# Performance work log

Measured on AMD Instinct MI355X. Metric: run time of the kernel, lower is better.

The kernel has to match this reference:

```python
import jax, jax.numpy as jnp
import numpy as np

B, S, D = 4, 2048, 1024
H = 16
HD = D // H  # head dim = 64


def setup_inputs() -> dict:
    key = jax.random.key(0)
    ks = jax.random.split(key, 9)
    s = 1.0 / np.sqrt(D)
    return {
        "Q": jax.random.normal(ks[0], (B, S, D), dtype=jnp.float32),
        "K": jax.random.normal(ks[1], (B, S, D), dtype=jnp.float32),
        "V": jax.random.normal(ks[2], (B, S, D), dtype=jnp.float32),
        "Wq": jax.random.uniform(ks[3], (D, D), jnp.float32, -s, s),
        "bq": jax.random.uniform(ks[4], (D,), jnp.float32, -s, s),
        "Wk": jax.random.uniform(ks[5], (D, D), jnp.float32, -s, s),
        "bk": jax.random.uniform(ks[6], (D,), jnp.float32, -s, s),
        "Wv": jax.random.uniform(ks[7], (D, D), jnp.float32, -s, s),
        "bv": jax.random.uniform(ks[8], (D,), jnp.float32, -s, s),
    }


def reference(Q, K, V, Wq, bq, Wk, bk, Wv, bv):
    # Linear projections, split into heads: (B, H, S, HD)
    def proj(x, W, b):
        y = x @ W + b  # torch Linear uses x @ W.T; here W is stored pre-transposed (D_in, D_out)
        return y.reshape(B, S, H, HD).transpose(0, 2, 1, 3)

    q = proj(Q, Wq, bq)
    k = proj(K, Wk, bk)
    v = proj(V, Wv, bv)

    scale = 1.0 / jnp.sqrt(jnp.float32(HD))
    scores = jnp.einsum("bhqd,bhkd->bhqk", q, k) * scale  # (B,H,S,S)
    # causal mask (mask=True path): -inf above the diagonal
    causal = jnp.triu(jnp.full((S, S), -jnp.inf, dtype=scores.dtype), k=1)
    scores = scores + causal
    attn = jax.nn.softmax(scores, axis=-1)
    ctx = jnp.einsum("bhqk,bhkd->bhqd", attn, v)  # (B,H,S,HD)
    return ctx.transpose(0, 2, 1, 3).reshape(B, S, H * HD)
```

## Files before the change

### kernel.cpp

```cpp
#include <hip/hip_runtime.h>
#include <hip/hip_bf16.h>
#include <stdint.h>

#define B_  4
#define S_  2048
#define D_  1024
#define H_  16
#define HD_ 64
#define LOG2E 1.44269504088896f

typedef unsigned short u16;
typedef short bf16x8 __attribute__((ext_vector_type(8)));
typedef float f32x4 __attribute__((ext_vector_type(4)));

static __device__ __forceinline__ u16 f2bf(float f) {
    union { float f; uint32_t u; } v; v.f = f;
    return (u16)((v.u + 0x7FFF + ((v.u >> 16) & 1)) >> 16);
}

static __device__ __forceinline__ uint32_t cvt_pk_bf16(float lo, float hi) {
    uint32_t r;
    asm("v_cvt_pk_bf16_f32 %0, %1, %2" : "=v"(r) : "v"(lo), "v"(hi));
    return r;
}

static __device__ __forceinline__ uint32_t pk2(float lo, float hi) {
    return __builtin_amdgcn_perm(__float_as_uint(hi), __float_as_uint(lo), 0x07060302u);
}

static __device__ __forceinline__ bf16x8 rd_swz(const u16* base, int row, int slot) {
    return *(const bf16x8*)((const char*)base + row * 128 + ((slot ^ (row & 7)) << 4));
}

static __device__ __forceinline__ void gll_swz(const u16* grow0, size_t stride,
                                               u16* lds_chunk, int lane) {
    const int r = lane >> 3;
    const int slot = (lane & 7) ^ r;
    const u16* g = grow0 + (size_t)r * stride + slot * 8;
    __builtin_amdgcn_global_load_lds(
        (const __attribute__((address_space(1))) uint32_t*)g,
        (__attribute__((address_space(3))) uint32_t*)lds_chunk, 16, 0, 0);
}

__global__ __launch_bounds__(256) void wtrans(
    const float* __restrict__ W0, const float* __restrict__ W1, const float* __restrict__ W2,
    u16* __restrict__ T0, u16* __restrict__ T1, u16* __restrict__ T2)
{
    const float* W = blockIdx.z == 0 ? W0 : (blockIdx.z == 1 ? W1 : W2);
    u16* T       = blockIdx.z == 0 ? T0 : (blockIdx.z == 1 ? T1 : T2);
    __shared__ float t[32][33];
    const int n0 = blockIdx.x * 32, k0 = blockIdx.y * 32;
    const int tx = threadIdx.x, ty = threadIdx.y;
#pragma unroll
    for (int i = 0; i < 4; ++i)
        t[ty + i * 8][tx] = W[(size_t)(k0 + ty + i * 8) * D_ + n0 + tx];
    __syncthreads();
#pragma unroll
    for (int i = 0; i < 4; ++i)
        T[(size_t)(n0 + ty + i * 8) * D_ + k0 + tx] = f2bf(t[tx][ty + i * 8]);
}

template <int MODE>
__global__ __launch_bounds__(256) void proj_gemm(
    const float* __restrict__ X, const u16* __restrict__ Wt,
    const float* __restrict__ bias, u16* __restrict__ out)
{
    __shared__ __align__(16) u16 lA[128 * 64];
    __shared__ __align__(16) u16 lB[128 * 64];
    const int tid = threadIdx.x;
    const int m0 = blockIdx.x * 128, n0 = blockIdx.y * 128;
    const int w = tid >> 6, lane = tid & 63;
    const int lr = lane & 15, lg = lane >> 4;
    const int wr = (w >> 1) * 64, wc = (w & 1) * 64;

    f32x4 acc[4][4] = {};

    for (int k0 = 0; k0 < D_; k0 += 64) {
        __syncthreads();
#pragma unroll
        for (int i = 0; i < 4; ++i) {
            const int c = w * 4 + i;
            gll_swz(Wt + (size_t)(n0 + c * 8) * D_ + k0, D_, &lB[c * 512], lane);
        }
#pragma unroll
        for (int i = 0; i < 8; ++i) {
            const int lin = i * 1024 + tid * 4;
            const int r = lin >> 6, c = lin & 63;
            const float4 v = *(const float4*)(X + (size_t)(m0 + r) * D_ + k0 + c);
            uint2 pk;
            pk.x = pk2(v.x, v.y);
            pk.y = pk2(v.z, v.w);
            const int phys = r * 128 + (((c >> 3) ^ (r & 7)) << 4) + ((c & 7) << 1);
            *(uint2*)((char*)lA + phys) = pk;
        }
        __syncthreads();
#pragma unroll
        for (int kk = 0; kk < 64; kk += 32) {
            bf16x8 af[4], bfr[4];
#pragma unroll
            for (int m = 0; m < 4; ++m)
                af[m] = rd_swz(lA, wr + m * 16 + lr, (kk >> 3) + lg);
#pragma unroll
            for (int n = 0; n < 4; ++n)
                bfr[n] = rd_swz(lB, wc + n * 16 + lr, (kk >> 3) + lg);
#pragma unroll
            for (int m = 0; m < 4; ++m)
#pragma unroll
                for (int n = 0; n < 4; ++n)
                    acc[m][n] = __builtin_amdgcn_mfma_f32_16x16x32_bf16(af[m], bfr[n], acc[m][n], 0, 0, 0);
        }
    }
#pragma unroll
    for (int m = 0; m < 4; ++m)
#pragma unroll
        for (int n = 0; n < 4; ++n)
#pragma unroll
            for (int j = 0; j < 4; ++j) {
                const int gm = m0 + wr + m * 16 + lg * 4 + j;
                const int gn = n0 + wc + n * 16 + lr;
                float y = acc[m][n][j] + bias[gn];
                if (MODE == 0) y *= 0.125f * LOG2E;
                const int bb = gm >> 11, s = gm & (S_ - 1);
                const int h = gn >> 6, hd = gn & 63;
                size_t off;
                if (MODE < 2) off = (((size_t)bb * H_ + h) * S_ + s) * HD_ + hd;
                else {
                    const int s6 = s & 63;
                    const int sp = (s & ~63) | (s6 & 0x20) | ((s6 & 0xC) << 1) |
                                   ((s6 & 0x10) >> 2) | (s6 & 3);
                    off = (((size_t)bb * H_ + h) * HD_ + hd) * S_ + sp;
                }
                out[off] = f2bf(y);
            }
}

__global__ __launch_bounds__(512) void attn_kernel(
    const u16* __restrict__ qb, const u16* __restrict__ kb,
    const u16* __restrict__ vtb, float* __restrict__ out)
{
    const int bh = blockIdx.y;
    const int b = bh >> 4, h = bh & 15;
    const int tid = threadIdx.x;
    const int w = tid >> 6, lane = tid & 63;
    const int lr = lane & 15, lg = lane >> 4;

    __shared__ __align__(16) u16 lK0[64 * 64];
    __shared__ __align__(16) u16 lV0[64 * 64];
    __shared__ __align__(16) u16 lK1[64 * 64];
    __shared__ __align__(16) u16 lV1[64 * 64];

    const size_t kbase = (size_t)bh * S_ * HD_;
    const size_t vbase = (size_t)bh * HD_ * S_;

    union { uint32_t u[4]; bf16x8 v; } onesf;
    onesf.u[0] = onesf.u[1] = onesf.u[2] = onesf.u[3] = 0x3F803F80u;

    for (int e = 0; e < 2; ++e) {
        const int qi = (e == 0) ? (int)blockIdx.x : 15 - (int)blockIdx.x;
        const int q0 = qi * 128;
        const int qrow = q0 + w * 16 + lr;

        const size_t qoff = ((size_t)bh * S_ + qrow) * HD_;
        const bf16x8 qf0 = *(const bf16x8*)(qb + qoff + lg * 8);
        const bf16x8 qf1 = *(const bf16x8*)(qb + qoff + 32 + lg * 8);

        f32x4 oacc[4] = {};
        f32x4 lacc = {};

        const int tmax = 2 * qi + 1;

        auto compute = [&](int t, const u16* lK, const u16* lV) {
            const int kv0 = t * 64;
            f32x4 sacc[4];
            __builtin_amdgcn_s_setprio(1);
#pragma unroll
            for (int n = 0; n < 4; ++n) {
                const bf16x8 k0f = rd_swz(lK, n * 16 + lr, lg);
                const bf16x8 k1f = rd_swz(lK, n * 16 + lr, 4 + lg);
                f32x4 z = {};
                z = __builtin_amdgcn_mfma_f32_16x16x32_bf16(k0f, qf0, z, 0, 0, 0);
                z = __builtin_amdgcn_mfma_f32_16x16x32_bf16(k1f, qf1, z, 0, 0, 0);
                sacc[n] = z;
            }
            __builtin_amdgcn_s_setprio(0);

            if (t >= tmax - 1) {
#pragma unroll
                for (int n = 0; n < 4; ++n)
#pragma unroll
                    for (int j = 0; j < 4; ++j)
                        if (kv0 + n * 16 + lg * 4 + j > qrow) sacc[n][j] = -1e30f;
            }

            uint32_t pw[4][2];
#pragma unroll
            for (int n = 0; n < 4; ++n)
#pragma unroll
                for (int jh = 0; jh < 2; ++jh)
                    pw[n][jh] = cvt_pk_bf16(exp2f(sacc[n][2 * jh]),
                                            exp2f(sacc[n][2 * jh + 1]));

            union { uint32_t u[4]; bf16x8 v; } a0, a1;
            a0.u[0] = pw[0][0]; a0.u[1] = pw[0][1];
            a0.u[2] = pw[1][0]; a0.u[3] = pw[1][1];
            a1.u[0] = pw[2][0]; a1.u[1] = pw[2][1];
            a1.u[2] = pw[3][0]; a1.u[3] = pw[3][1];

            __builtin_amdgcn_s_setprio(1);
#pragma unroll
            for (int n = 0; n < 4; ++n) {
                const int row = n * 16 + lr;
                const bf16x8 vf0 = rd_swz(lV, row, lg);
                const bf16x8 vf1 = rd_swz(lV, row, 4 + lg);
                oacc[n] = __builtin_amdgcn_mfma_f32_16x16x32_bf16(a0.v, vf0, oacc[n], 0, 0, 0);
                oacc[n] = __builtin_amdgcn_mfma_f32_16x16x32_bf16(a1.v, vf1, oacc[n], 0, 0, 0);
            }
            lacc = __builtin_amdgcn_mfma_f32_16x16x32_bf16(a0.v, onesf.v, lacc, 0, 0, 0);
            lacc = __builtin_amdgcn_mfma_f32_16x16x32_bf16(a1.v, onesf.v, lacc, 0, 0, 0);
            __builtin_amdgcn_s_setprio(0);
        };

        for (int tp = 0; tp <= tmax; tp += 2) {
            const int kvA = tp * 64, kvB = kvA + 64;
            __syncthreads();
            gll_swz(kb + kbase + (size_t)(kvA + w * 8) * HD_, HD_, &lK0[w * 512], lane);
            gll_swz(vtb + vbase + (size_t)(w * 8) * S_ + kvA, S_, &lV0[w * 512], lane);
            gll_swz(kb + kbase + (size_t)(kvB + w * 8) * HD_, HD_, &lK1[w * 512], lane);
            gll_swz(vtb + vbase + (size_t)(w * 8) * S_ + kvB, S_, &lV1[w * 512], lane);
            __syncthreads();

            compute(tp, lK0, lV0);
            if (!(tp + 1 == tmax && w < 4)) compute(tp + 1, lK1, lV1);
        }

        f32x4 inv;
#pragma unroll
        for (int j = 0; j < 4; ++j) inv[j] = 1.f / lacc[j];
#pragma unroll
        for (int j = 0; j < 4; ++j) {
            const int row = q0 + w * 16 + lg * 4 + j;
#pragma unroll
            for (int n = 0; n < 4; ++n)
                out[((size_t)b * S_ + row) * D_ + h * HD_ + n * 16 + lr] = oacc[n][j] * inv[j];
        }
    }
}

extern "C" void kernel_launch(void* const* d_in, const int* in_sizes, int n_in,
                              void* d_out, int out_size, void* d_ws, size_t ws_size,
                              hipStream_t stream) {
    const float* Q  = (const float*)d_in[0];
    const float* K  = (const float*)d_in[1];
    const float* V  = (const float*)d_in[2];
    const float* Wq = (const float*)d_in[3];
    const float* bq = (const float*)d_in[4];
    const float* Wk = (const float*)d_in[5];
    const float* bk = (const float*)d_in[6];
    const float* Wv = (const float*)d_in[7];
    const float* bv = (const float*)d_in[8];
    float* out = (float*)d_out;

    char* ws = (char*)d_ws;
    const size_t WT_BYTES  = (size_t)D_ * D_ * 2;
    const size_t QKV_BYTES = (size_t)B_ * S_ * D_ * 2;
    u16* Wtq = (u16*)(ws);
    u16* Wtk = (u16*)(ws + WT_BYTES);
    u16* Wtv = (u16*)(ws + 2 * WT_BYTES);
    u16* qb  = (u16*)(ws + 3 * WT_BYTES);
    u16* kb  = (u16*)(ws + 3 * WT_BYTES + QKV_BYTES);
    u16* vtb = (u16*)(ws + 3 * WT_BYTES + 2 * QKV_BYTES);

    wtrans<<<dim3(32, 32, 3), dim3(32, 8), 0, stream>>>(Wq, Wk, Wv, Wtq, Wtk, Wtv);
    proj_gemm<0><<<dim3(64, 8), dim3(256), 0, stream>>>(Q, Wtq, bq, qb);
    proj_gemm<1><<<dim3(64, 8), dim3(256), 0, stream>>>(K, Wtk, bk, kb);
    proj_gemm<2><<<dim3(64, 8), dim3(256), 0, stream>>>(V, Wtv, bv, vtb);
    attn_kernel<<<dim3(8, B_ * H_), dim3(512), 0, stream>>>(qb, kb, vtb, out);
}
```

Measured before the change: 154.9 us.

## Double-buffer LDS in projection GEMM and attention to overlap loads with MFMA

Both the projection GEMM and the attention kernel now use two LDS buffers. The next K-tile (or KV pair) is prefetched while the current one is computed, which removes one barrier per iteration. In the GEMM, the fp32 activations are held in registers and converted to bf16 into the alternate buffer after the MFMAs. This costs twice the LDS (64KB per block in both kernels) and more VGPRs, which may lower occupancy. Correctness depends on the gll_swz async loads being waited on before the single barrier.

```diff
diff --git a/kernel.cpp b/kernel.cpp
--- a/kernel.cpp
+++ b/kernel.cpp
@@ -65,8 +65,8 @@
     const float* __restrict__ X, const u16* __restrict__ Wt,
     const float* __restrict__ bias, u16* __restrict__ out)
 {
-    __shared__ __align__(16) u16 lA[128 * 64];
-    __shared__ __align__(16) u16 lB[128 * 64];
+    __shared__ __align__(16) u16 lA[2][128 * 64];
+    __shared__ __align__(16) u16 lB[2][128 * 64];
     const int tid = threadIdx.x;
     const int m0 = blockIdx.x * 128, n0 = blockIdx.y * 128;
     const int w = tid >> 6, lane = tid & 63;
@@ -74,42 +74,69 @@
     const int wr = (w >> 1) * 64, wc = (w & 1) * 64;
 
     f32x4 acc[4][4] = {};
-
-    for (int k0 = 0; k0 < D_; k0 += 64) {
-        __syncthreads();
-#pragma unroll
-        for (int i = 0; i < 4; ++i) {
-            const int c = w * 4 + i;
-            gll_swz(Wt + (size_t)(n0 + c * 8) * D_ + k0, D_, &lB[c * 512], lane);
-        }
+    float4 areg[8];
+
+    auto loadA = [&](int k0) {
 #pragma unroll
         for (int i = 0; i < 8; ++i) {
             const int lin = i * 1024 + tid * 4;
             const int r = lin >> 6, c = lin & 63;
-            const float4 v = *(const float4*)(X + (size_t)(m0 + r) * D_ + k0 + c);
+            areg[i] = *(const float4*)(X + (size_t)(m0 + r) * D_ + k0 + c);
+        }
+    };
+    auto writeA = [&](u16* dst) {
+#pragma unroll
+        for (int i = 0; i < 8; ++i) {
+            const int lin = i * 1024 + tid * 4;
+            const int r = lin >> 6, c = lin & 63;
             uint2 pk;
-            pk.x = pk2(v.x, v.y);
-            pk.y = pk2(v.z, v.w);
+            pk.x = pk2(areg[i].x, areg[i].y);
+            pk.y = pk2(areg[i].z, areg[i].w);
             const int phys = r * 128 + (((c >> 3) ^ (r & 7)) << 4) + ((c & 7) << 1);
-            *(uint2*)((char*)lA + phys) = pk;
-        }
-        __syncthreads();
-#pragma unroll
-        for (int kk = 0; kk < 64; kk += 32) {
+            *(uint2*)((char*)dst + phys) = pk;
+        }
+    };
+    auto stageB = [&](int k0, u16* dst) {
+#pragma unroll
+        for (int i = 0; i < 4; ++i) {
+            const int c = w * 4 + i;
+            gll_swz(Wt + (size_t)(n0 + c * 8) * D_ + k0, D_, dst + c * 512, lane);
+        }
+    };
+    auto mfmaStep = [&](const u16* A, const u16* Bb) {
+#pragma unroll
+        for (int kk = 0; kk < 2; ++kk) {
             bf16x8 af[4], bfr[4];
 #pragma unroll
             for (int m = 0; m < 4; ++m)
-                af[m] = rd_swz(lA, wr + m * 16 + lr, (kk >> 3) + lg);
+                af[m] = rd_swz(A, wr + m * 16 + lr, kk * 4 + lg);
 #pragma unroll
             for (int n = 0; n < 4; ++n)
-                bfr[n] = rd_swz(lB, wc + n * 16 + lr, (kk >> 3) + lg);
+                bfr[n] = rd_swz(Bb, wc + n * 16 + lr, kk * 4 + lg);
 #pragma unroll
             for (int m = 0; m < 4; ++m)
 #pragma unroll
                 for (int n = 0; n < 4; ++n)
                     acc[m][n] = __builtin_amdgcn_mfma_f32_16x16x32_bf16(af[m], bfr[n], acc[m][n], 0, 0, 0);
         }
+    };
+
+    loadA(0);
+    stageB(0, lB[0]);
+    writeA(lA[0]);
+    __syncthreads();
+
+    for (int k0 = 0, s = 0; k0 < D_; k0 += 64, s ^= 1) {
+        const int nk = k0 + 64;
+        if (nk < D_) {
+            loadA(nk);
+            stageB(nk, lB[s ^ 1]);
+        }
+        mfmaStep(lA[s], lB[s]);
+        if (nk < D_) writeA(lA[s ^ 1]);
+        __syncthreads();
     }
+
 #pragma unroll
     for (int m = 0; m < 4; ++m)
 #pragma unroll
@@ -120,13 +147,13 @@
                 const int gn = n0 + wc + n * 16 + lr;
                 float y = acc[m][n][j] + bias[gn];
                 if (MODE == 0) y *= 0.125f * LOG2E;
-                const int bb = gm >> 11, s = gm & (S_ - 1);
+                const int bb = gm >> 11, s2 = gm & (S_ - 1);
                 const int h = gn >> 6, hd = gn & 63;
                 size_t off;
-                if (MODE < 2) off = (((size_t)bb * H_ + h) * S_ + s) * HD_ + hd;
+                if (MODE < 2) off = (((size_t)bb * H_ + h) * S_ + s2) * HD_ + hd;
                 else {
-                    const int s6 = s & 63;
-                    const int sp = (s & ~63) | (s6 & 0x20) | ((s6 & 0xC) << 1) |
+                    const int s6 = s2 & 63;
+                    const int sp = (s2 & ~63) | (s6 & 0x20) | ((s6 & 0xC) << 1) |
                                    ((s6 & 0x10) >> 2) | (s6 & 3);
                     off = (((size_t)bb * H_ + h) * HD_ + hd) * S_ + sp;
                 }
@@ -144,10 +171,7 @@
     const int w = tid >> 6, lane = tid & 63;
     const int lr = lane & 15, lg = lane >> 4;
 
-    __shared__ __align__(16) u16 lK0[64 * 64];
-    __shared__ __align__(16) u16 lV0[64 * 64];
-    __shared__ __align__(16) u16 lK1[64 * 64];
-    __shared__ __align__(16) u16 lV1[64 * 64];
+    __shared__ __align__(16) u16 lds[2][4][64 * 64];
 
     const size_t kbase = (size_t)bh * S_ * HD_;
     const size_t vbase = (size_t)bh * HD_ * S_;
@@ -168,6 +192,15 @@
         f32x4 lacc = {};
 
         const int tmax = 2 * qi + 1;
+
+        auto stage = [&](int tp, int s) {
+            const int kvA = tp * 64, kvB = kvA + 64;
+            u16* d = &lds[s][0][0];
+            gll_swz(kb + kbase + (size_t)(kvA + w * 8) * HD_, HD_, d + w * 512, lane);
+            gll_swz(vtb + vbase + (size_t)(w * 8) * S_ + kvA, S_, d + 4096 + w * 512, lane);
+            gll_swz(kb + kbase + (size_t)(kvB + w * 8) * HD_, HD_, d + 8192 + w * 512, lane);
+            gll_swz(vtb + vbase + (size_t)(w * 8) * S_ + kvB, S_, d + 12288 + w * 512, lane);
+        };
 
         auto compute = [&](int t, const u16* lK, const u16* lV) {
             const int kv0 = t * 64;
@@ -220,17 +253,15 @@
             __builtin_amdgcn_s_setprio(0);
         };
 
-        for (int tp = 0; tp <= tmax; tp += 2) {
-            const int kvA = tp * 64, kvB = kvA + 64;
+        stage(0, 0);
+        __syncthreads();
+
+        for (int tp = 0, s = 0; tp <= tmax; tp += 2, s ^= 1) {
+            if (tp + 2 <= tmax) stage(tp + 2, s ^ 1);
+            const u16* base = &lds[s][0][0];
+            compute(tp, base, base + 4096);
+            if (!(tp + 1 == tmax && w < 4)) compute(tp + 1, base + 8192, base + 12288);
             __syncthreads();
-            gll_swz(kb + kbase + (size_t)(kvA + w * 8) * HD_, HD_, &lK0[w * 512], lane);
-            gll_swz(vtb + vbase + (size_t)(w * 8) * S_ + kvA, S_, &lV0[w * 512], lane);
-            gll_swz(kb + kbase + (size_t)(kvB + w * 8) * HD_, HD_, &lK1[w * 512], lane);
-            gll_swz(vtb + vbase + (size_t)(w * 8) * S_ + kvB, S_, &lV1[w * 512], lane);
-            __syncthreads();
-
-            compute(tp, lK0, lV0);
-            if (!(tp + 1 == tmax && w < 4)) compute(tp + 1, lK1, lV1);
         }
 
         f32x4 inv;
```

Result: faster. 150.8 us (-2.7%).

## Double-buffer attention K/V staging and enlarge projection GEMM M tile

Applied to the files above, without the earlier changes.

The attention kernel now uses two LDS stages so the next pair of K/V tiles is loaded while the current pair is computed, with a single barrier per iteration. The goal is to hide global-to-LDS load latency that the old load-sync-compute loop exposed. The projection GEMM tile grows from 128 to 256 rows, giving 8x4 accumulators per wave and halving the grid. That improves weight-tile reuse but raises register pressure and leaves only 256 blocks per projection, which may underfill the GPU.

```diff
diff --git a/kernel.cpp b/kernel.cpp
--- a/kernel.cpp
+++ b/kernel.cpp
@@ -65,15 +65,15 @@
     const float* __restrict__ X, const u16* __restrict__ Wt,
     const float* __restrict__ bias, u16* __restrict__ out)
 {
-    __shared__ __align__(16) u16 lA[128 * 64];
+    __shared__ __align__(16) u16 lA[256 * 64];
     __shared__ __align__(16) u16 lB[128 * 64];
     const int tid = threadIdx.x;
-    const int m0 = blockIdx.x * 128, n0 = blockIdx.y * 128;
+    const int m0 = blockIdx.x * 256, n0 = blockIdx.y * 128;
     const int w = tid >> 6, lane = tid & 63;
     const int lr = lane & 15, lg = lane >> 4;
-    const int wr = (w >> 1) * 64, wc = (w & 1) * 64;
-
-    f32x4 acc[4][4] = {};
+    const int wr = (w >> 1) * 128, wc = (w & 1) * 64;
+
+    f32x4 acc[8][4] = {};
 
     for (int k0 = 0; k0 < D_; k0 += 64) {
         __syncthreads();
@@ -83,7 +83,7 @@
             gll_swz(Wt + (size_t)(n0 + c * 8) * D_ + k0, D_, &lB[c * 512], lane);
         }
 #pragma unroll
-        for (int i = 0; i < 8; ++i) {
+        for (int i = 0; i < 16; ++i) {
             const int lin = i * 1024 + tid * 4;
             const int r = lin >> 6, c = lin & 63;
             const float4 v = *(const float4*)(X + (size_t)(m0 + r) * D_ + k0 + c);
@@ -95,23 +95,23 @@
         }
         __syncthreads();
 #pragma unroll
-        for (int kk = 0; kk < 64; kk += 32) {
-            bf16x8 af[4], bfr[4];
-#pragma unroll
-            for (int m = 0; m < 4; ++m)
-                af[m] = rd_swz(lA, wr + m * 16 + lr, (kk >> 3) + lg);
+        for (int kk = 0; kk < 2; ++kk) {
+            bf16x8 af[8], bfr[4];
+#pragma unroll
+            for (int m = 0; m < 8; ++m)
+                af[m] = rd_swz(lA, wr + m * 16 + lr, kk * 4 + lg);
 #pragma unroll
             for (int n = 0; n < 4; ++n)
-                bfr[n] = rd_swz(lB, wc + n * 16 + lr, (kk >> 3) + lg);
-#pragma unroll
-            for (int m = 0; m < 4; ++m)
+                bfr[n] = rd_swz(lB, wc + n * 16 + lr, kk * 4 + lg);
+#pragma unroll
+            for (int m = 0; m < 8; ++m)
 #pragma unroll
                 for (int n = 0; n < 4; ++n)
                     acc[m][n] = __builtin_amdgcn_mfma_f32_16x16x32_bf16(af[m], bfr[n], acc[m][n], 0, 0, 0);
         }
     }
 #pragma unroll
-    for (int m = 0; m < 4; ++m)
+    for (int m = 0; m < 8; ++m)
 #pragma unroll
         for (int n = 0; n < 4; ++n)
 #pragma unroll
@@ -120,13 +120,13 @@
                 const int gn = n0 + wc + n * 16 + lr;
                 float y = acc[m][n][j] + bias[gn];
                 if (MODE == 0) y *= 0.125f * LOG2E;
-                const int bb = gm >> 11, s = gm & (S_ - 1);
+                const int bb = gm >> 11, s2 = gm & (S_ - 1);
                 const int h = gn >> 6, hd = gn & 63;
                 size_t off;
-                if (MODE < 2) off = (((size_t)bb * H_ + h) * S_ + s) * HD_ + hd;
+                if (MODE < 2) off = (((size_t)bb * H_ + h) * S_ + s2) * HD_ + hd;
                 else {
-                    const int s6 = s & 63;
-                    const int sp = (s & ~63) | (s6 & 0x20) | ((s6 & 0xC) << 1) |
+                    const int s6 = s2 & 63;
+                    const int sp = (s2 & ~63) | (s6 & 0x20) | ((s6 & 0xC) << 1) |
                                    ((s6 & 0x10) >> 2) | (s6 & 3);
                     off = (((size_t)bb * H_ + h) * HD_ + hd) * S_ + sp;
                 }
@@ -144,10 +144,7 @@
     const int w = tid >> 6, lane = tid & 63;
     const int lr = lane & 15, lg = lane >> 4;
 
-    __shared__ __align__(16) u16 lK0[64 * 64];
-    __shared__ __align__(16) u16 lV0[64 * 64];
-    __shared__ __align__(16) u16 lK1[64 * 64];
-    __shared__ __align__(16) u16 lV1[64 * 64];
+    __shared__ __align__(16) u16 lds[2][4][64 * 64];
 
     const size_t kbase = (size_t)bh * S_ * HD_;
     const size_t vbase = (size_t)bh * HD_ * S_;
@@ -168,6 +165,15 @@
         f32x4 lacc = {};
 
         const int tmax = 2 * qi + 1;
+
+        auto stage = [&](int tp, int s) {
+            const int kvA = tp * 64, kvB = kvA + 64;
+            u16* d = &lds[s][0][0];
+            gll_swz(kb + kbase + (size_t)(kvA + w * 8) * HD_, HD_, d + w * 512, lane);
+            gll_swz(vtb + vbase + (size_t)(w * 8) * S_ + kvA, S_, d + 4096 + w * 512, lane);
+            gll_swz(kb + kbase + (size_t)(kvB + w * 8) * HD_, HD_, d + 8192 + w * 512, lane);
+            gll_swz(vtb + vbase + (size_t)(w * 8) * S_ + kvB, S_, d + 12288 + w * 512, lane);
+        };
 
         auto compute = [&](int t, const u16* lK, const u16* lV) {
             const int kv0 = t * 64;
@@ -220,17 +226,15 @@
             __builtin_amdgcn_s_setprio(0);
         };
 
-        for (int tp = 0; tp <= tmax; tp += 2) {
-            const int kvA = tp * 64, kvB = kvA + 64;
+        stage(0, 0);
+        __syncthreads();
+
+        for (int tp = 0, s = 0; tp <= tmax; tp += 2, s ^= 1) {
+            if (tp + 2 <= tmax) stage(tp + 2, s ^ 1);
+            const u16* base = &lds[s][0][0];
+            compute(tp, base, base + 4096);
+            if (!(tp + 1 == tmax && w < 4)) compute(tp + 1, base + 8192, base + 12288);
             __syncthreads();
-            gll_swz(kb + kbase + (size_t)(kvA + w * 8) * HD_, HD_, &lK0[w * 512], lane);
-            gll_swz(vtb + vbase + (size_t)(w * 8) * S_ + kvA, S_, &lV0[w * 512], lane);
-            gll_swz(kb + kbase + (size_t)(kvB + w * 8) * HD_, HD_, &lK1[w * 512], lane);
-            gll_swz(vtb + vbase + (size_t)(w * 8) * S_ + kvB, S_, &lV1[w * 512], lane);
-            __syncthreads();
-
-            compute(tp, lK0, lV0);
-            if (!(tp + 1 == tmax && w < 4)) compute(tp + 1, lK1, lV1);
         }
 
         f32x4 inv;
@@ -271,8 +275,8 @@
     u16* vtb = (u16*)(ws + 3 * WT_BYTES + 2 * QKV_BYTES);
 
     wtrans<<<dim3(32, 32, 3), dim3(32, 8), 0, stream>>>(Wq, Wk, Wv, Wtq, Wtk, Wtv);
-    proj_gemm<0><<<dim3(64, 8), dim3(256), 0, stream>>>(Q, Wtq, bq, qb);
-    proj_gemm<1><<<dim3(64, 8), dim3(256), 0, stream>>>(K, Wtk, bk, kb);
-    proj_gemm<2><<<dim3(64, 8), dim3(256), 0, stream>>>(V, Wtv, bv, vtb);
+    proj_gemm<0><<<dim3(32, 8), dim3(256), 0, stream>>>(Q, Wtq, bq, qb);
+    proj_gemm<1><<<dim3(32, 8), dim3(256), 0, stream>>>(K, Wtk, bk, kb);
+    proj_gemm<2><<<dim3(32, 8), dim3(256), 0, stream>>>(V, Wtv, bv, vtb);
     attn_kernel<<<dim3(8, B_ * H_), dim3(512), 0, stream>>>(qb, kb, vtb, out);
 }
```

New measurement: 188.4 us. 21.6% more time.
